# Kernel tuning notes

Measured on AMD Instinct MI355X. Metric: run time of the kernel, lower is better.

The kernel has to match this reference:

```python
import jax, jax.numpy as jnp
import numpy as np

D = 128
H = 128  # scorer hidden

def setup_inputs() -> dict:
    key = jax.random.key(0)
    ks = jax.random.split(key, 8)
    B, T = 4096, 200
    transformer_out = jax.random.normal(ks[0], (B, T, D), dtype=jnp.float32)
    candidate = jax.random.normal(ks[1], (B, D), dtype=jnp.float32)
    mask = jax.random.randint(ks[2], (B, T), 0, 2).astype(jnp.bool_)
    # scorer params: Linear(3D,H) -> PReLU -> Linear(H,1)
    lim1 = 1.0 / np.sqrt(3 * D)
    W1 = jax.random.uniform(ks[3], (3 * D, H), minval=-lim1, maxval=lim1, dtype=jnp.float32)
    b1 = jax.random.uniform(ks[4], (H,), minval=-lim1, maxval=lim1, dtype=jnp.float32)
    a = jnp.array(0.25, dtype=jnp.float32)  # PReLU default init
    lim2 = 1.0 / np.sqrt(H)
    W2 = jax.random.uniform(ks[5], (H, 1), minval=-lim2, maxval=lim2, dtype=jnp.float32)
    b2 = jax.random.uniform(ks[6], (1,), minval=-lim2, maxval=lim2, dtype=jnp.float32)
    return {"transformer_out": transformer_out, "candidate": candidate, "mask": mask,
            "W1": W1, "b1": b1, "a": a, "W2": W2, "b2": b2}

def reference(transformer_out, candidate, mask, W1, b1, a, W2, b2):
    # transformer_out: [B,T,D], candidate: [B,D]
    cand_exp = jnp.broadcast_to(candidate[:, None, :], transformer_out.shape)  # [B,T,D]
    att_input = jnp.concatenate([transformer_out, cand_exp, transformer_out * cand_exp], axis=-1)  # [B,T,3D]
    h = att_input @ W1 + b1                       # [B,T,H]
    h = jnp.where(h >= 0, h, a * h)               # PReLU (single shared alpha)
    scores = (h @ W2 + b2)[..., 0]                # [B,T]
    scores = jnp.where(mask, scores, -jnp.inf)
    weights = jax.nn.softmax(scores, axis=-1)     # [B,T]
    return jnp.einsum('bt,btd->bd', weights, transformer_out)  # [B,D]
```

## Files before the change

### kernel.cpp

```cpp
#include <hip/hip_runtime.h>
#include <hip/hip_bf16.h>

typedef __attribute__((ext_vector_type(8))) short short8;
typedef __attribute__((ext_vector_type(4))) float f32x4;

#define B_T 200
#define B_D 128

static __device__ __forceinline__ short f2bf(float f) {
  unsigned u = __builtin_bit_cast(unsigned, f);
  u += 0x7fffu + ((u >> 16) & 1u);
  return (short)(u >> 16);
}
static __device__ __forceinline__ float bf2f(short s) {
  unsigned u = ((unsigned)(unsigned short)s) << 16;
  return __builtin_bit_cast(float, u);
}

__global__ __launch_bounds__(512, 4)
void ta_fused(const float* __restrict__ x,
              const float* __restrict__ cand,
              const void*  __restrict__ maskp,
              const float* __restrict__ W1,
              const float* __restrict__ b1,
              const float* __restrict__ ap,
              const float* __restrict__ W2,
              const float* __restrict__ b2p,
              float* __restrict__ out)
{
  __shared__ __align__(16) short wbt[B_D * B_D];
  __shared__ float c_lds[B_D];
  __shared__ float w2_lds[B_D];
  __shared__ float beta_lds[B_D];
  __shared__ float part[8][B_D];
  __shared__ float scores[208];
  __shared__ float red[16];
  __shared__ int flag1b;

  const int b    = blockIdx.x;
  const int tid  = threadIdx.x;
  const int lane = tid & 63;
  const int wv   = tid >> 6;
  const int l15  = lane & 15;
  const int g    = lane >> 4;

  if (tid == 0) flag1b = 0;
  __syncthreads();

  {
    const unsigned char* mb = (const unsigned char*)maskp;
    int local = 0;
    #pragma unroll
    for (int i = 0; i < 8; ++i) {
      int idx = tid * 8 + i;
      if ((idx & 3) != 0 && mb[idx] != 0) local = 1;
    }
    if (local) flag1b = 1;
  }
  if (tid < B_D) {
    c_lds[tid]  = cand[(size_t)b * B_D + tid];
    w2_lds[tid] = W2[tid];
  }
  __syncthreads();

  #pragma unroll 4
  for (int it = 0; it < 16; ++it) {
    int item = it * 512 + tid;
    int j  = item & 127;
    int kp = item >> 7;
    int k0 = kp * 2;
    float c0 = c_lds[k0], c1 = c_lds[k0 + 1];
    float wa0 = W1[(size_t)k0 * B_D + j];
    float wc0 = W1[(size_t)(256 + k0) * B_D + j];
    float wa1 = W1[(size_t)(k0 + 1) * B_D + j];
    float wc1 = W1[(size_t)(256 + k0 + 1) * B_D + j];
    unsigned lo = (unsigned short)f2bf(wa0 + c0 * wc0);
    unsigned hi = (unsigned short)f2bf(wa1 + c1 * wc1);
    ((unsigned*)wbt)[((k0 >> 3) * B_D + j) * 4 + ((k0 & 7) >> 1)] = lo | (hi << 16);
  }
  {
    int j = tid & 127, kh = tid >> 7;
    float s = 0.f;
    const float* w1b = W1 + (size_t)(B_D + kh * 32) * B_D + j;
    #pragma unroll 4
    for (int k = 0; k < 32; ++k) s += c_lds[kh * 32 + k] * w1b[(size_t)k * B_D];
    part[kh][j] = s;
  }
  __syncthreads();
  if (tid < B_D) beta_lds[tid] = b1[tid] + part[0][tid] + part[1][tid] + part[2][tid] + part[3][tid];
  __syncthreads();

  float betaL[8], w2L[8];
  #pragma unroll
  for (int nt = 0; nt < 8; ++nt) {
    int col = nt * 16 + l15;
    betaL[nt] = beta_lds[col];
    w2L[nt]   = w2_lds[col];
  }
  const float alpha = ap[0];
  const float b2    = b2p[0];

  const int ntile = (wv < 5) ? 2 : 1;
  short8 af[2][4];

  #pragma unroll
  for (int ti = 0; ti < 2; ++ti) {
    if (ti < ntile) {
      const int mt = wv + ti * 8;
      int row = mt * 16 + l15; if (row > B_T - 1) row = B_T - 1;
      const float* xr = x + ((size_t)b * B_T + row) * B_D + g * 8;
      #pragma unroll
      for (int ks = 0; ks < 4; ++ks) {
        float4 f0 = *(const float4*)(xr + ks * 32);
        float4 f1 = *(const float4*)(xr + ks * 32 + 4);
        short8 t;
        t[0]=f2bf(f0.x); t[1]=f2bf(f0.y); t[2]=f2bf(f0.z); t[3]=f2bf(f0.w);
        t[4]=f2bf(f1.x); t[5]=f2bf(f1.y); t[6]=f2bf(f1.z); t[7]=f2bf(f1.w);
        af[ti][ks] = t;
      }
    }
  }
  #pragma unroll
  for (int ti = 0; ti < 2; ++ti) {
    if (ti < ntile) {
      const int mt = wv + ti * 8;
      const int tb = mt * 16;
      float sc[4] = {0.f, 0.f, 0.f, 0.f};
      #pragma unroll
      for (int nt = 0; nt < 8; ++nt) {
        f32x4 acc = {0.f, 0.f, 0.f, 0.f};
        #pragma unroll
        for (int ks = 0; ks < 4; ++ks) {
          short8 bf = *(const short8*)&wbt[(((ks * 4 + g) * B_D) + nt * 16 + l15) * 8];
          acc = __builtin_amdgcn_mfma_f32_16x16x32_bf16(af[ti][ks], bf, acc, 0, 0, 0);
        }
        #pragma unroll
        for (int r = 0; r < 4; ++r) {
          float h = acc[r] + betaL[nt];
          float p = (h >= 0.f) ? h : alpha * h;
          sc[r] += p * w2L[nt];
        }
      }
      #pragma unroll
      for (int r = 0; r < 4; ++r) {
        float v = sc[r];
        v += __shfl_xor(v, 1, 16);
        v += __shfl_xor(v, 2, 16);
        v += __shfl_xor(v, 4, 16);
        v += __shfl_xor(v, 8, 16);
        if (l15 == 0) scores[tb + g * 4 + r] = v + b2;
      }
    }
  }
  __syncthreads();

  {
    const int t = tid;
    bool mk = false;
    float s = -INFINITY;
    if (t < B_T) {
      if (flag1b) mk = ((const unsigned char*)maskp)[(size_t)b * B_T + t] != 0;
      else        mk = ((const int*)maskp)[(size_t)b * B_T + t] != 0;
      if (mk) s = scores[t];
    }
    float v = s;
    #pragma unroll
    for (int m = 32; m >= 1; m >>= 1) v = fmaxf(v, __shfl_xor(v, m, 64));
    if (lane == 0) red[wv] = v;
    __syncthreads();
    float mx = -INFINITY;
    #pragma unroll
    for (int i = 0; i < 8; ++i) mx = fmaxf(mx, red[i]);
    float e = (t < B_T && mk) ? __expf(s - mx) : 0.f;
    float sv = e;
    #pragma unroll
    for (int m = 32; m >= 1; m >>= 1) sv += __shfl_xor(sv, m, 64);
    if (lane == 0) red[8 + wv] = sv;
    __syncthreads();
    float Z = 0.f;
    #pragma unroll
    for (int i = 0; i < 8; ++i) Z += red[8 + i];
    float w = e / Z;
    if (t < 208) scores[t] = w;
  }
  __syncthreads();

  {
    float w0 = scores[(wv + 0 * 8) * 16 + l15];
    float w1 = (ntile > 1) ? scores[(wv + 1 * 8) * 16 + l15] : 0.f;
    #pragma unroll
    for (int ks = 0; ks < 4; ++ks) {
      float accw[8];
      #pragma unroll
      for (int e = 0; e < 8; ++e) accw[e] = 0.f;
      {
        short8 t0 = af[0][ks];
        #pragma unroll
        for (int e = 0; e < 8; ++e) accw[e] += w0 * bf2f(t0[e]);
      }
      if (ntile > 1) {
        short8 t1 = af[1][ks];
        #pragma unroll
        for (int e = 0; e < 8; ++e) accw[e] += w1 * bf2f(t1[e]);
      }
      #pragma unroll
      for (int e = 0; e < 8; ++e) {
        float v = accw[e];
        v += __shfl_xor(v, 1, 16);
        v += __shfl_xor(v, 2, 16);
        v += __shfl_xor(v, 4, 16);
        v += __shfl_xor(v, 8, 16);
        if (l15 == 0) part[wv][ks * 32 + g * 8 + e] = v;
      }
    }
  }
  __syncthreads();
  if (tid < B_D) {
    float s = 0.f;
    #pragma unroll
    for (int i = 0; i < 8; ++i) s += part[i][tid];
    out[(size_t)b * B_D + tid] = s;
  }
}

extern "C" void kernel_launch(void* const* d_in, const int* in_sizes, int n_in,
                              void* d_out, int out_size, void* d_ws, size_t ws_size,
                              hipStream_t stream) {
  const float* x    = (const float*)d_in[0];
  const float* cand = (const float*)d_in[1];
  const void*  mask = d_in[2];
  const float* W1   = (const float*)d_in[3];
  const float* b1   = (const float*)d_in[4];
  const float* a    = (const float*)d_in[5];
  const float* W2   = (const float*)d_in[6];
  const float* b2   = (const float*)d_in[7];
  float* out = (float*)d_out;
  const int B = in_sizes[1] / B_D;
  ta_fused<<<B, 512, 0, stream>>>(x, cand, mask, W1, b1, a, W2, b2, out);
}
```

Baseline: 167.8 us.

## Issue activation loads first and cut barriers in the fused attention kernel

The x row loads for both tiles now go out at kernel start, before the per-batch weight folding, so global memory latency overlaps with the W1/candidate precompute. The mask-format detection uses a wave-level __any over a 64-bit load instead of a shared flag with two barriers, and the mask value is fetched early. The candidate is read directly from global memory, and the bias reduction is folded into the register loads, which removes two __syncthreads. The cost is higher register pressure from holding 16 float4 values in flight, and tile-1 rows for waves 5-7 are now always loaded and converted (clamped to valid rows, weighted by zero).

```diff
diff --git a/kernel.cpp b/kernel.cpp
--- a/kernel.cpp
+++ b/kernel.cpp
@@ -15,6 +15,12 @@
 static __device__ __forceinline__ float bf2f(short s) {
   unsigned u = ((unsigned)(unsigned short)s) << 16;
   return __builtin_bit_cast(float, u);
+}
+static __device__ __forceinline__ short8 cvt8(f32x4 a, f32x4 b) {
+  short8 t;
+  t[0] = f2bf(a[0]); t[1] = f2bf(a[1]); t[2] = f2bf(a[2]); t[3] = f2bf(a[3]);
+  t[4] = f2bf(b[0]); t[5] = f2bf(b[1]); t[6] = f2bf(b[2]); t[7] = f2bf(b[3]);
+  return t;
 }
 
 __global__ __launch_bounds__(512, 4)
@@ -29,13 +35,11 @@
               float* __restrict__ out)
 {
   __shared__ __align__(16) short wbt[B_D * B_D];
-  __shared__ float c_lds[B_D];
+  __shared__ float part[4][B_D];
   __shared__ float w2_lds[B_D];
-  __shared__ float beta_lds[B_D];
-  __shared__ float part[8][B_D];
+  __shared__ float pout[8][B_D];
   __shared__ float scores[208];
   __shared__ float red[16];
-  __shared__ int flag1b;
 
   const int b    = blockIdx.x;
   const int tid  = threadIdx.x;
@@ -44,125 +48,105 @@
   const int l15  = lane & 15;
   const int g    = lane >> 4;
 
-  if (tid == 0) flag1b = 0;
-  __syncthreads();
-
+  const int row0 = wv * 16 + l15;
+  int row1 = (8 + wv) * 16 + l15; if (row1 > B_T - 1) row1 = B_T - 1;
+  const float* xr0 = x + ((size_t)b * B_T + row0) * B_D + g * 8;
+  const float* xr1 = x + ((size_t)b * B_T + row1) * B_D + g * 8;
+  f32x4 r00 = *(const f32x4*)(xr0 +  0), r01 = *(const f32x4*)(xr0 +  4);
+  f32x4 r02 = *(const f32x4*)(xr0 + 32), r03 = *(const f32x4*)(xr0 + 36);
+  f32x4 r04 = *(const f32x4*)(xr0 + 64), r05 = *(const f32x4*)(xr0 + 68);
+  f32x4 r06 = *(const f32x4*)(xr0 + 96), r07 = *(const f32x4*)(xr0 + 100);
+  f32x4 r10 = *(const f32x4*)(xr1 +  0), r11 = *(const f32x4*)(xr1 +  4);
+  f32x4 r12 = *(const f32x4*)(xr1 + 32), r13 = *(const f32x4*)(xr1 + 36);
+  f32x4 r14 = *(const f32x4*)(xr1 + 64), r15 = *(const f32x4*)(xr1 + 68);
+  f32x4 r16 = *(const f32x4*)(xr1 + 96), r17 = *(const f32x4*)(xr1 + 100);
+
+  int flag1b;
   {
     const unsigned char* mb = (const unsigned char*)maskp;
-    int local = 0;
-    #pragma unroll
-    for (int i = 0; i < 8; ++i) {
-      int idx = tid * 8 + i;
-      if ((idx & 3) != 0 && mb[idx] != 0) local = 1;
+    unsigned long long v8 = *(const unsigned long long*)(mb + lane * 8);
+    flag1b = __any((v8 & 0xFFFFFF00FFFFFF00ull) != 0ull);
+  }
+  bool mk = false;
+  if (tid < B_T) {
+    if (flag1b) mk = ((const unsigned char*)maskp)[(size_t)b * B_T + tid] != 0;
+    else        mk = ((const int*)maskp)[(size_t)b * B_T + tid] != 0;
+  }
+
+  if (tid < B_D) w2_lds[tid] = W2[tid];
+
+  const float* cb = cand + (size_t)b * B_D;
+  {
+    const int j  = tid & 127;
+    const int q  = tid >> 7;
+    #pragma unroll 4
+    for (int it = 0; it < 16; ++it) {
+      int k0 = it * 8 + q * 2;
+      float c0 = cb[k0], c1 = cb[k0 + 1];
+      float wa0 = W1[(size_t)k0 * B_D + j];
+      float wc0 = W1[(size_t)(256 + k0) * B_D + j];
+      float wa1 = W1[(size_t)(k0 + 1) * B_D + j];
+      float wc1 = W1[(size_t)(256 + k0 + 1) * B_D + j];
+      unsigned lo = (unsigned short)f2bf(wa0 + c0 * wc0);
+      unsigned hi = (unsigned short)f2bf(wa1 + c1 * wc1);
+      ((unsigned*)wbt)[((k0 >> 3) * B_D + j) * 4 + ((k0 & 7) >> 1)] = lo | (hi << 16);
     }
-    if (local) flag1b = 1;
-  }
-  if (tid < B_D) {
-    c_lds[tid]  = cand[(size_t)b * B_D + tid];
-    w2_lds[tid] = W2[tid];
-  }
-  __syncthreads();
-
-  #pragma unroll 4
-  for (int it = 0; it < 16; ++it) {
-    int item = it * 512 + tid;
-    int j  = item & 127;
-    int kp = item >> 7;
-    int k0 = kp * 2;
-    float c0 = c_lds[k0], c1 = c_lds[k0 + 1];
-    float wa0 = W1[(size_t)k0 * B_D + j];
-    float wc0 = W1[(size_t)(256 + k0) * B_D + j];
-    float wa1 = W1[(size_t)(k0 + 1) * B_D + j];
-    float wc1 = W1[(size_t)(256 + k0 + 1) * B_D + j];
-    unsigned lo = (unsigned short)f2bf(wa0 + c0 * wc0);
-    unsigned hi = (unsigned short)f2bf(wa1 + c1 * wc1);
-    ((unsigned*)wbt)[((k0 >> 3) * B_D + j) * 4 + ((k0 & 7) >> 1)] = lo | (hi << 16);
-  }
-  {
-    int j = tid & 127, kh = tid >> 7;
-    float s = 0.f;
-    const float* w1b = W1 + (size_t)(B_D + kh * 32) * B_D + j;
+    float s = (q == 0) ? b1[j] : 0.f;
+    const float* w1b = W1 + (size_t)(B_D + q * 32) * B_D + j;
     #pragma unroll 4
-    for (int k = 0; k < 32; ++k) s += c_lds[kh * 32 + k] * w1b[(size_t)k * B_D];
-    part[kh][j] = s;
-  }
-  __syncthreads();
-  if (tid < B_D) beta_lds[tid] = b1[tid] + part[0][tid] + part[1][tid] + part[2][tid] + part[3][tid];
+    for (int k = 0; k < 32; ++k) s += cb[q * 32 + k] * w1b[(size_t)k * B_D];
+    part[q][j] = s;
+  }
   __syncthreads();
 
   float betaL[8], w2L[8];
   #pragma unroll
   for (int nt = 0; nt < 8; ++nt) {
     int col = nt * 16 + l15;
-    betaL[nt] = beta_lds[col];
+    betaL[nt] = part[0][col] + part[1][col] + part[2][col] + part[3][col];
     w2L[nt]   = w2_lds[col];
   }
   const float alpha = ap[0];
   const float b2    = b2p[0];
 
+  short8 af00 = cvt8(r00, r01), af01 = cvt8(r02, r03);
+  short8 af02 = cvt8(r04, r05), af03 = cvt8(r06, r07);
+  short8 af10 = cvt8(r10, r11), af11 = cvt8(r12, r13);
+  short8 af12 = cvt8(r14, r15), af13 = cvt8(r16, r17);
+
+#define TILE_SCORE(A0, A1, A2, A3, TB) do {                                   \
+    float sc[4] = {0.f, 0.f, 0.f, 0.f};                                       \
+    _Pragma("unroll")                                                         \
+    for (int nt = 0; nt < 8; ++nt) {                                          \
+      f32x4 acc = {0.f, 0.f, 0.f, 0.f};                                       \
+      const short8* wp = (const short8*)wbt + g * B_D + nt * 16 + l15;        \
+      acc = __builtin_amdgcn_mfma_f32_16x16x32_bf16(A0, wp[0],    acc, 0,0,0);\
+      acc = __builtin_amdgcn_mfma_f32_16x16x32_bf16(A1, wp[512],  acc, 0,0,0);\
+      acc = __builtin_amdgcn_mfma_f32_16x16x32_bf16(A2, wp[1024], acc, 0,0,0);\
+      acc = __builtin_amdgcn_mfma_f32_16x16x32_bf16(A3, wp[1536], acc, 0,0,0);\
+      _Pragma("unroll")                                                       \
+      for (int r = 0; r < 4; ++r) {                                           \
+        float h = acc[r] + betaL[nt];                                         \
+        float p = (h >= 0.f) ? h : alpha * h;                                 \
+        sc[r] += p * w2L[nt];                                                 \
+      }                                                                       \
+    }                                                                         \
+    _Pragma("unroll")                                                         \
+    for (int r = 0; r < 4; ++r) {                                             \
+      float v = sc[r];                                                        \
+      v += __shfl_xor(v, 1, 16); v += __shfl_xor(v, 2, 16);                   \
+      v += __shfl_xor(v, 4, 16); v += __shfl_xor(v, 8, 16);                   \
+      if (l15 == 0) scores[(TB) + g * 4 + r] = v + b2;                        \
+    }                                                                         \
+  } while (0)
+
   const int ntile = (wv < 5) ? 2 : 1;
-  short8 af[2][4];
-
-  #pragma unroll
-  for (int ti = 0; ti < 2; ++ti) {
-    if (ti < ntile) {
-      const int mt = wv + ti * 8;
-      int row = mt * 16 + l15; if (row > B_T - 1) row = B_T - 1;
-      const float* xr = x + ((size_t)b * B_T + row) * B_D + g * 8;
-      #pragma unroll
-      for (int ks = 0; ks < 4; ++ks) {
-        float4 f0 = *(const float4*)(xr + ks * 32);
-        float4 f1 = *(const float4*)(xr + ks * 32 + 4);
-        short8 t;
-        t[0]=f2bf(f0.x); t[1]=f2bf(f0.y); t[2]=f2bf(f0.z); t[3]=f2bf(f0.w);
-        t[4]=f2bf(f1.x); t[5]=f2bf(f1.y); t[6]=f2bf(f1.z); t[7]=f2bf(f1.w);
-        af[ti][ks] = t;
-      }
-    }
-  }
-  #pragma unroll
-  for (int ti = 0; ti < 2; ++ti) {
-    if (ti < ntile) {
-      const int mt = wv + ti * 8;
-      const int tb = mt * 16;
-      float sc[4] = {0.f, 0.f, 0.f, 0.f};
-      #pragma unroll
-      for (int nt = 0; nt < 8; ++nt) {
-        f32x4 acc = {0.f, 0.f, 0.f, 0.f};
-        #pragma unroll
-        for (int ks = 0; ks < 4; ++ks) {
-          short8 bf = *(const short8*)&wbt[(((ks * 4 + g) * B_D) + nt * 16 + l15) * 8];
-          acc = __builtin_amdgcn_mfma_f32_16x16x32_bf16(af[ti][ks], bf, acc, 0, 0, 0);
-        }
-        #pragma unroll
-        for (int r = 0; r < 4; ++r) {
-          float h = acc[r] + betaL[nt];
-          float p = (h >= 0.f) ? h : alpha * h;
-          sc[r] += p * w2L[nt];
-        }
-      }
-      #pragma unroll
-      for (int r = 0; r < 4; ++r) {
-        float v = sc[r];
-        v += __shfl_xor(v, 1, 16);
-        v += __shfl_xor(v, 2, 16);
-        v += __shfl_xor(v, 4, 16);
-        v += __shfl_xor(v, 8, 16);
-        if (l15 == 0) scores[tb + g * 4 + r] = v + b2;
-      }
-    }
-  }
-  __syncthreads();
-
-  {
-    const int t = tid;
-    bool mk = false;
-    float s = -INFINITY;
-    if (t < B_T) {
-      if (flag1b) mk = ((const unsigned char*)maskp)[(size_t)b * B_T + t] != 0;
-      else        mk = ((const int*)maskp)[(size_t)b * B_T + t] != 0;
-      if (mk) s = scores[t];
-    }
+  TILE_SCORE(af00, af01, af02, af03, wv * 16);
+  if (ntile > 1) TILE_SCORE(af10, af11, af12, af13, (8 + wv) * 16);
+  __syncthreads();
+
+  {
+    float s = (tid < B_T && mk) ? scores[tid] : -INFINITY;
     float v = s;
     #pragma unroll
     for (int m = 32; m >= 1; m >>= 1) v = fmaxf(v, __shfl_xor(v, m, 64));
@@ -171,7 +155,7 @@
     float mx = -INFINITY;
     #pragma unroll
     for (int i = 0; i < 8; ++i) mx = fmaxf(mx, red[i]);
-    float e = (t < B_T && mk) ? __expf(s - mx) : 0.f;
+    float e = mk ? __expf(s - mx) : 0.f;
     float sv = e;
     #pragma unroll
     for (int m = 32; m >= 1; m >>= 1) sv += __shfl_xor(sv, m, 64);
@@ -180,37 +164,26 @@
     float Z = 0.f;
     #pragma unroll
     for (int i = 0; i < 8; ++i) Z += red[8 + i];
-    float w = e / Z;
-    if (t < 208) scores[t] = w;
-  }
-  __syncthreads();
-
-  {
-    float w0 = scores[(wv + 0 * 8) * 16 + l15];
-    float w1 = (ntile > 1) ? scores[(wv + 1 * 8) * 16 + l15] : 0.f;
+    if (tid < 208) scores[tid] = e / Z;
+  }
+  __syncthreads();
+
+  {
+    float w0 = scores[wv * 16 + l15];
+    float w1 = (ntile > 1) ? scores[(8 + wv) * 16 + l15] : 0.f;
     #pragma unroll
     for (int ks = 0; ks < 4; ++ks) {
+      short8 t0 = (ks == 0) ? af00 : (ks == 1) ? af01 : (ks == 2) ? af02 : af03;
+      short8 t1 = (ks == 0) ? af10 : (ks == 1) ? af11 : (ks == 2) ? af12 : af13;
       float accw[8];
       #pragma unroll
-      for (int e = 0; e < 8; ++e) accw[e] = 0.f;
-      {
-        short8 t0 = af[0][ks];
-        #pragma unroll
-        for (int e = 0; e < 8; ++e) accw[e] += w0 * bf2f(t0[e]);
-      }
-      if (ntile > 1) {
-        short8 t1 = af[1][ks];
-        #pragma unroll
-        for (int e = 0; e < 8; ++e) accw[e] += w1 * bf2f(t1[e]);
-      }
+      for (int e = 0; e < 8; ++e) accw[e] = w0 * bf2f(t0[e]) + w1 * bf2f(t1[e]);
       #pragma unroll
       for (int e = 0; e < 8; ++e) {
         float v = accw[e];
-        v += __shfl_xor(v, 1, 16);
-        v += __shfl_xor(v, 2, 16);
-        v += __shfl_xor(v, 4, 16);
-        v += __shfl_xor(v, 8, 16);
-        if (l15 == 0) part[wv][ks * 32 + g * 8 + e] = v;
+        v += __shfl_xor(v, 1, 16); v += __shfl_xor(v, 2, 16);
+        v += __shfl_xor(v, 4, 16); v += __shfl_xor(v, 8, 16);
+        if (l15 == 0) pout[wv][ks * 32 + g * 8 + e] = v;
       }
     }
   }
@@ -218,7 +191,7 @@
   if (tid < B_D) {
     float s = 0.f;
     #pragma unroll
-    for (int i = 0; i < 8; ++i) s += part[i][tid];
+    for (int i = 0; i < 8; ++i) s += pout[i][tid];
     out[(size_t)b * B_D + tid] = s;
   }
 }
```

Result: slower. 260.2 us (+55.0%).
